# Kernel tuning notes

Measured on AMD Instinct MI355X. Metric: run time of the kernel, lower is better.

## Reference

```python
import jax, jax.numpy as jnp
import numpy as np

# LSNNParameters defaults (norse-style)
ALPHA = 100.0            # surrogate sharpness
DT = 1e-3
TAU_SYN_INV = 1.0 / 0.005   # 200
TAU_MEM_INV = 1.0 / 0.01    # 100
TAU_ADAPT_INV = 1.0 / 800.0
V_LEAK = 0.0
V_RESET = 0.0
BETA = 1.8
VTH = 1.0                # sp.vth_init / v_th default


@jax.custom_vjp
def superspike(x):
    # Heaviside forward, SuperSpike surrogate backward ('super' method)
    return (x > 0).astype(x.dtype)

def _ss_fwd(x):
    return superspike(x), x

def _ss_bwd(x, g):
    return (g / (ALPHA * jnp.abs(x) + 1.0) ** 2,)

superspike.defvjp(_ss_fwd, _ss_bwd)


def lsnn_scan(x, w_in, w_rec):
    # x: [T, B, N_in]; w_in: [H, N_in]; w_rec: [H, H]
    T, B, _ = x.shape
    H = w_in.shape[0]
    z0 = jnp.zeros((B, H), x.dtype)
    v0 = jnp.full((B, H), V_LEAK, x.dtype)
    i0 = jnp.zeros((B, H), x.dtype)
    b0 = jnp.full((B, H), VTH, x.dtype)  # mean(v_th)

    def step(carry, xt):
        z, v, i, b = carry
        v_dec = v + DT * TAU_MEM_INV * (V_LEAK - v + i)
        i_dec = i - DT * TAU_SYN_INV * i
        b_dec = b + DT * TAU_ADAPT_INV * (VTH - b)
        z_new = superspike(v_dec - b_dec)
        zd = jax.lax.stop_gradient(z_new)  # reset/adaptation use detached spike
        v_new = (1.0 - zd) * v_dec + zd * V_RESET
        i_new = i_dec + xt @ w_in.T + z @ w_rec.T
        b_new = b_dec + zd * BETA
        return (z_new, v_new, i_new, b_new), z_new

    (zf, vf, i_f, bf), outs = jax.lax.scan(step, (z0, v0, i0, b0), x)
    return outs, (zf, vf, i_f, bf)


def setup_inputs() -> dict:
    key = jax.random.key(0)
    k1, k2, k3 = jax.random.split(key, 3)
    T, B, N_IN, H = 512, 64, 512, 1024
    x = jax.random.normal(k1, (T, B, N_IN), jnp.float32)
    w_in = jax.random.normal(k2, (H, N_IN), jnp.float32) * np.float32(np.sqrt(2.0 / H))
    w_rec = jax.random.normal(k3, (H, H), jnp.float32) * np.float32(np.sqrt(2.0 / H))
    w_rec = w_rec * (1.0 - jnp.eye(H, dtype=jnp.float32))  # autapses=False
    return {"input_tensor": x, "input_weights": w_in, "recurrent_weights": w_rec}


def reference(input_tensor, input_weights, recurrent_weights):
    return lsnn_scan(input_tensor, input_weights, recurrent_weights)
```

## Files before the change

kernel.cpp:

```cpp
#include <hip/hip_runtime.h>

typedef float f32x4 __attribute__((ext_vector_type(4)));

#define T_STEPS 512
#define BATCH   64
#define NIN     512
#define H       1024
#define BH      (BATCH * H)

#define BM 128
#define BN 128
#define BK 16
#define LDSS 132

__global__ void transpose1024(const float* __restrict__ in, float* __restrict__ out) {
    __shared__ float tile[32][33];
    const int tx = threadIdx.x, ty = threadIdx.y;
    const int xg = blockIdx.x * 32 + tx;
    const int ybase = blockIdx.y * 32;
#pragma unroll
    for (int r = 0; r < 32; r += 8)
        tile[ty + r][tx] = in[(size_t)(ybase + ty + r) * H + xg];
    __syncthreads();
    const int x2 = blockIdx.y * 32 + tx;
    const int y2base = blockIdx.x * 32;
#pragma unroll
    for (int r = 0; r < 32; r += 8)
        out[(size_t)(y2base + ty + r) * H + x2] = tile[tx][ty + r];
}

__global__ __launch_bounds__(256) void gemm_xwin(const float* __restrict__ x,
                                                 const float* __restrict__ w,
                                                 float* __restrict__ cur) {
    __shared__ __align__(16) float As[BK][LDSS];
    __shared__ __align__(16) float Bs[BK][LDSS];
    const int tid = threadIdx.x;
    const int tx = tid & 15, ty = tid >> 4;
    const int tx4 = tx * 4, ty4 = ty * 4;
    const int m0 = blockIdx.y * BM;
    const int n0 = blockIdx.x * BN;

    float acc[8][8];
#pragma unroll
    for (int i = 0; i < 8; ++i)
#pragma unroll
        for (int j = 0; j < 8; ++j) acc[i][j] = 0.0f;

    const int ar = tid >> 2;
    const int akc = (tid & 3) * 4;

    float4 a0 = *reinterpret_cast<const float4*>(&x[(size_t)(m0 + ar) * NIN + akc]);
    float4 a1 = *reinterpret_cast<const float4*>(&x[(size_t)(m0 + ar + 64) * NIN + akc]);
    float4 b0 = *reinterpret_cast<const float4*>(&w[(size_t)(n0 + ar) * NIN + akc]);
    float4 b1 = *reinterpret_cast<const float4*>(&w[(size_t)(n0 + ar + 64) * NIN + akc]);

    for (int k0 = 0; k0 < NIN; k0 += BK) {
        __syncthreads();
        As[akc + 0][ar] = a0.x; As[akc + 1][ar] = a0.y; As[akc + 2][ar] = a0.z; As[akc + 3][ar] = a0.w;
        As[akc + 0][ar + 64] = a1.x; As[akc + 1][ar + 64] = a1.y; As[akc + 2][ar + 64] = a1.z; As[akc + 3][ar + 64] = a1.w;
        Bs[akc + 0][ar] = b0.x; Bs[akc + 1][ar] = b0.y; Bs[akc + 2][ar] = b0.z; Bs[akc + 3][ar] = b0.w;
        Bs[akc + 0][ar + 64] = b1.x; Bs[akc + 1][ar + 64] = b1.y; Bs[akc + 2][ar + 64] = b1.z; Bs[akc + 3][ar + 64] = b1.w;
        __syncthreads();

        const int kn = (k0 + BK < NIN) ? (k0 + BK) : 0;
        a0 = *reinterpret_cast<const float4*>(&x[(size_t)(m0 + ar) * NIN + kn + akc]);
        a1 = *reinterpret_cast<const float4*>(&x[(size_t)(m0 + ar + 64) * NIN + kn + akc]);
        b0 = *reinterpret_cast<const float4*>(&w[(size_t)(n0 + ar) * NIN + kn + akc]);
        b1 = *reinterpret_cast<const float4*>(&w[(size_t)(n0 + ar + 64) * NIN + kn + akc]);

#pragma unroll
        for (int kk = 0; kk < BK; ++kk) {
            const float4 av0 = *reinterpret_cast<const float4*>(&As[kk][ty4]);
            const float4 av1 = *reinterpret_cast<const float4*>(&As[kk][ty4 + 64]);
            const float4 bv0 = *reinterpret_cast<const float4*>(&Bs[kk][tx4]);
            const float4 bv1 = *reinterpret_cast<const float4*>(&Bs[kk][tx4 + 64]);
            const float ar_[8] = {av0.x, av0.y, av0.z, av0.w, av1.x, av1.y, av1.z, av1.w};
            const float br_[8] = {bv0.x, bv0.y, bv0.z, bv0.w, bv1.x, bv1.y, bv1.z, bv1.w};
#pragma unroll
            for (int i = 0; i < 8; ++i)
#pragma unroll
                for (int j = 0; j < 8; ++j)
                    acc[i][j] = fmaf(ar_[i], br_[j], acc[i][j]);
        }
    }

#pragma unroll
    for (int gi = 0; gi < 2; ++gi)
#pragma unroll
        for (int ii = 0; ii < 4; ++ii) {
            const int i = gi * 4 + ii;
            const int row = m0 + ty4 + ii + gi * 64;
            float* dst = &cur[(size_t)row * H + n0 + tx4];
            *reinterpret_cast<float4*>(dst)      = make_float4(acc[i][0], acc[i][1], acc[i][2], acc[i][3]);
            *reinterpret_cast<float4*>(dst + 64) = make_float4(acc[i][4], acc[i][5], acc[i][6], acc[i][7]);
        }
}

__global__ __launch_bounds__(256, 1) void lsnn_scan_kernel(float* __restrict__ io,
                                                           const float* __restrict__ wrecT) {
    const int tid = threadIdx.x;
    const int wave = tid >> 6, lane = tid & 63;
    const int j0 = tid * 4;
    const int wq = wave * 256;
    const int b = blockIdx.x;

    __shared__ __align__(16) float ring[3][4][1024];
    __shared__ __align__(16) int list[2][1088];
    __shared__ __align__(16) int cnt[2][4];

    float sv0 = 0.f, sv1 = 0.f, sv2 = 0.f, sv3 = 0.f;
    float si0 = 0.f, si1 = 0.f, si2 = 0.f, si3 = 0.f;
    float sb0 = 1.f, sb1 = 1.f, sb2 = 1.f, sb3 = 1.f;
    float sz0 = 0.f, sz1 = 0.f, sz2 = 0.f, sz3 = 0.f;
    int p = 0;
    int n_carry = 0;

    const float C_MEM = (float)(1e-3 * 100.0);
    const float C_SYN = (float)(1e-3 * 200.0);
    const float C_AD  = (float)(1e-3 * (1.0 / 800.0));
    const float BETA  = 1.8f;

    float* base = io + (size_t)b * H + j0;

    f32x4 P0 = *reinterpret_cast<const f32x4*>(base + (size_t)0 * BH);
    f32x4 P1 = *reinterpret_cast<const f32x4*>(base + (size_t)1 * BH);
    f32x4 P2 = *reinterpret_cast<const f32x4*>(base + (size_t)2 * BH);
    f32x4 P3 = *reinterpret_cast<const f32x4*>(base + (size_t)3 * BH);
    f32x4 P4 = *reinterpret_cast<const f32x4*>(base + (size_t)4 * BH);
    f32x4 P5 = *reinterpret_cast<const f32x4*>(base + (size_t)5 * BH);
    f32x4 P6 = *reinterpret_cast<const f32x4*>(base + (size_t)6 * BH);
    f32x4 P7 = *reinterpret_cast<const f32x4*>(base + (size_t)7 * BH);

#define STAGE(G, SLOT)                                                        \
  { const int A0s_ = (G) << 2;                                                \
    _Pragma("unroll")                                                         \
    for (int rr_ = 0; rr_ < 4; ++rr_) {                                       \
      const int ps_ = A0s_ + rr_;                                             \
      int hs_ = lst[ps_];                                                     \
      hs_ = (ps_ < n) ? hs_ : 0;                                              \
      const float* gp_ = wrecT + (size_t)(unsigned)hs_ * H + wq + lane * 4;   \
      __builtin_amdgcn_global_load_lds(                                       \
          (const __attribute__((address_space(1))) unsigned int*)gp_,         \
          (__attribute__((address_space(3))) unsigned int*)&ring[SLOT][rr_][wq], \
          16, 0, 0);                                                          \
    } }

#define SCAN_STEP(T, CREG, PF)                                                \
  {                                                                           \
    const float cc0 = CREG.x, cc1 = CREG.y, cc2 = CREG.z, cc3 = CREG.w;       \
    const int n = __builtin_amdgcn_readfirstlane(n_carry);                    \
    const int NT = (n + 3) >> 2;                                              \
    const int* lst = &list[p][0];                                             \
     \
    if (NT > 0) STAGE(0, 0);                                                  \
    if (NT > 1) STAGE(1, 1);                                                  \
    if (NT > 2) STAGE(2, 2);                                                  \
                                  \
    const float vd0 = sv0 + C_MEM * (0.0f - sv0 + si0);                       \
    const float vd1 = sv1 + C_MEM * (0.0f - sv1 + si1);                       \
    const float vd2 = sv2 + C_MEM * (0.0f - sv2 + si2);                       \
    const float vd3 = sv3 + C_MEM * (0.0f - sv3 + si3);                       \
    const float id0 = si0 - C_SYN * si0;                                      \
    const float id1 = si1 - C_SYN * si1;                                      \
    const float id2 = si2 - C_SYN * si2;                                      \
    const float id3 = si3 - C_SYN * si3;                                      \
    const float bd0 = sb0 + C_AD * (1.0f - sb0);                              \
    const float bd1 = sb1 + C_AD * (1.0f - sb1);                              \
    const float bd2 = sb2 + C_AD * (1.0f - sb2);                              \
    const float bd3 = sb3 + C_AD * (1.0f - sb3);                              \
    sz0 = ((vd0 - bd0) > 0.0f) ? 1.0f : 0.0f;                                 \
    sz1 = ((vd1 - bd1) > 0.0f) ? 1.0f : 0.0f;                                 \
    sz2 = ((vd2 - bd2) > 0.0f) ? 1.0f : 0.0f;                                 \
    sz3 = ((vd3 - bd3) > 0.0f) ? 1.0f : 0.0f;                                 \
    sv0 = (sz0 > 0.0f) ? 0.0f : vd0;                                          \
    sv1 = (sz1 > 0.0f) ? 0.0f : vd1;                                          \
    sv2 = (sz2 > 0.0f) ? 0.0f : vd2;                                          \
    sv3 = (sz3 > 0.0f) ? 0.0f : vd3;                                          \
    sb0 = (sz0 > 0.0f) ? (bd0 + BETA) : bd0;                                  \
    sb1 = (sz1 > 0.0f) ? (bd1 + BETA) : bd1;                                  \
    sb2 = (sz2 > 0.0f) ? (bd2 + BETA) : bd2;                                  \
    sb3 = (sz3 > 0.0f) ? (bd3 + BETA) : bd3;                                  \
    *reinterpret_cast<f32x4*>(base + (size_t)(T) * BH) =                      \
        (f32x4){sz0, sz1, sz2, sz3};                                          \
    const unsigned long long m0 = __ballot(sz0 > 0.0f);                       \
    const unsigned long long m1 = __ballot(sz1 > 0.0f);                       \
    const unsigned long long m2 = __ballot(sz2 > 0.0f);                       \
    const unsigned long long m3 = __ballot(sz3 > 0.0f);                       \
    unsigned pos = __builtin_amdgcn_mbcnt_hi((unsigned)(m0 >> 32),            \
                   __builtin_amdgcn_mbcnt_lo((unsigned)m0, 0u));              \
    pos = __builtin_amdgcn_mbcnt_hi((unsigned)(m1 >> 32),                     \
          __builtin_amdgcn_mbcnt_lo((unsigned)m1, pos));                      \
    pos = __builtin_amdgcn_mbcnt_hi((unsigned)(m2 >> 32),                     \
          __builtin_amdgcn_mbcnt_lo((unsigned)m2, pos));                      \
    pos = __builtin_amdgcn_mbcnt_hi((unsigned)(m3 >> 32),                     \
          __builtin_amdgcn_mbcnt_lo((unsigned)m3, pos));                      \
    if (lane == 0)                                                            \
      cnt[p ^ 1][wave] = __popcll(m0) + __popcll(m1) + __popcll(m2) + __popcll(m3); \
    asm volatile("s_waitcnt lgkmcnt(0)" ::: "memory");                        \
    __builtin_amdgcn_s_barrier();                                             \
    const int4 nc = *reinterpret_cast<const int4*>(&cnt[p ^ 1][0]);           \
    n_carry = nc.x + nc.y + nc.z + nc.w;                                      \
    const int woff = (wave > 0 ? nc.x : 0) + (wave > 1 ? nc.y : 0) +          \
                     (wave > 2 ? nc.z : 0);                                   \
    int* dst = &list[p ^ 1][woff];                                            \
    if (sz0 > 0.0f) dst[pos++] = j0 + 0;                                      \
    if (sz1 > 0.0f) dst[pos++] = j0 + 1;                                      \
    if (sz2 > 0.0f) dst[pos++] = j0 + 2;                                      \
    if (sz3 > 0.0f) dst[pos++] = j0 + 3;                                      \
    asm volatile("s_waitcnt lgkmcnt(0)" ::: "memory");                        \
    __builtin_amdgcn_s_barrier();                                             \
        \
    float r0 = 0.f, r1 = 0.f, r2 = 0.f, r3 = 0.f;                             \
    {                                                                         \
      int sl = 0;                                                             \
      for (int g = 0; g < NT; ++g) {                                          \
        const int rem = NT - 1 - g;                                           \
        if (rem >= 2)      { asm volatile("s_waitcnt vmcnt(8)" ::: "memory"); } \
        else if (rem == 1) { asm volatile("s_waitcnt vmcnt(4)" ::: "memory"); } \
        else               { asm volatile("s_waitcnt vmcnt(0)" ::: "memory"); } \
        const f32x4 w0 = *reinterpret_cast<const f32x4*>(&ring[sl][0][j0]);   \
        const f32x4 w1 = *reinterpret_cast<const f32x4*>(&ring[sl][1][j0]);   \
        const f32x4 w2 = *reinterpret_cast<const f32x4*>(&ring[sl][2][j0]);   \
        const f32x4 w3 = *reinterpret_cast<const f32x4*>(&ring[sl][3][j0]);   \
        const int gb = g << 2;                                                \
        if (gb + 4 <= n) {                                                    \
          r0 += w0.x; r1 += w0.y; r2 += w0.z; r3 += w0.w;                     \
          r0 += w1.x; r1 += w1.y; r2 += w1.z; r3 += w1.w;                     \
          r0 += w2.x; r1 += w2.y; r2 += w2.z; r3 += w2.w;                     \
          r0 += w3.x; r1 += w3.y; r2 += w3.z; r3 += w3.w;                     \
        } else {                                                              \
          const float ma_ = (gb + 0 < n) ? 1.0f : 0.0f;                       \
          r0 = fmaf(ma_, w0.x, r0); r1 = fmaf(ma_, w0.y, r1);                 \
          r2 = fmaf(ma_, w0.z, r2); r3 = fmaf(ma_, w0.w, r3);                 \
          const float mb_ = (gb + 1 < n) ? 1.0f : 0.0f;                       \
          r0 = fmaf(mb_, w1.x, r0); r1 = fmaf(mb_, w1.y, r1);                 \
          r2 = fmaf(mb_, w1.z, r2); r3 = fmaf(mb_, w1.w, r3);                 \
          const float mc_ = (gb + 2 < n) ? 1.0f : 0.0f;                       \
          r0 = fmaf(mc_, w2.x, r0); r1 = fmaf(mc_, w2.y, r1);                 \
          r2 = fmaf(mc_, w2.z, r2); r3 = fmaf(mc_, w2.w, r3);                 \
          const float md_ = (gb + 3 < n) ? 1.0f : 0.0f;                       \
          r0 = fmaf(md_, w3.x, r0); r1 = fmaf(md_, w3.y, r1);                 \
          r2 = fmaf(md_, w3.z, r2); r3 = fmaf(md_, w3.w, r3);                 \
        }                                                                     \
        if (g + 3 < NT) {                                                     \
             \
          asm volatile("s_waitcnt lgkmcnt(0)" ::: "memory");                  \
          STAGE(g + 3, sl);                                                   \
        }                                                                     \
        sl = (sl == 2) ? 0 : sl + 1;                                          \
      }                                                                       \
    }                                                                         \
    if (PF) {                                                                 \
      if ((T) + 1 < T_STEPS) {                                                \
        const float* pb = base + (size_t)((T) + 1) * BH;                      \
        P0 = *(const f32x4*)(pb + (size_t)0 * BH);                            \
        P1 = *(const f32x4*)(pb + (size_t)1 * BH);                            \
        P2 = *(const f32x4*)(pb + (size_t)2 * BH);                            \
        P3 = *(const f32x4*)(pb + (size_t)3 * BH);                            \
        P4 = *(const f32x4*)(pb + (size_t)4 * BH);                            \
        P5 = *(const f32x4*)(pb + (size_t)5 * BH);                            \
        P6 = *(const f32x4*)(pb + (size_t)6 * BH);                            \
        P7 = *(const f32x4*)(pb + (size_t)7 * BH);                            \
      }                                                                       \
    }                                                                         \
    si0 = (id0 + cc0) + r0;                                                   \
    si1 = (id1 + cc1) + r1;                                                   \
    si2 = (id2 + cc2) + r2;                                                   \
    si3 = (id3 + cc3) + r3;                                                   \
    p ^= 1;                                                                   \
  }

    for (int t = 0; t < T_STEPS; t += 8) {
        SCAN_STEP(t,     P0, 0);
        SCAN_STEP(t + 1, P1, 0);
        SCAN_STEP(t + 2, P2, 0);
        SCAN_STEP(t + 3, P3, 0);
        SCAN_STEP(t + 4, P4, 0);
        SCAN_STEP(t + 5, P5, 0);
        SCAN_STEP(t + 6, P6, 0);
        SCAN_STEP(t + 7, P7, 1);
    }
#undef SCAN_STEP
#undef STAGE

    float* fo = io + (size_t)T_STEPS * BH + (size_t)b * H + j0;
    *reinterpret_cast<float4*>(fo)          = make_float4(sz0, sz1, sz2, sz3);
    *reinterpret_cast<float4*>(fo + BH)     = make_float4(sv0, sv1, sv2, sv3);
    *reinterpret_cast<float4*>(fo + 2 * BH) = make_float4(si0, si1, si2, si3);
    *reinterpret_cast<float4*>(fo + 3 * BH) = make_float4(sb0, sb1, sb2, sb3);
}

extern "C" void kernel_launch(void* const* d_in, const int* in_sizes, int n_in,
                              void* d_out, int out_size, void* d_ws, size_t ws_size,
                              hipStream_t stream) {
    const float* x     = (const float*)d_in[0];
    const float* w_in  = (const float*)d_in[1];
    const float* w_rec = (const float*)d_in[2];
    float* out   = (float*)d_out;
    float* wrecT = (float*)d_ws;

    transpose1024<<<dim3(H / 32, H / 32), dim3(32, 8), 0, stream>>>(w_rec, wrecT);
    gemm_xwin<<<dim3(H / BN, (T_STEPS * BATCH) / BM), 256, 0, stream>>>(x, w_in, out);
    lsnn_scan_kernel<<<BATCH, 256, 0, stream>>>(out, wrecT);
}
```

Measured before the change: 747.9 us.

## Overlap tail of input GEMM with recurrent scan using persistent fused kernel

The input projection GEMM is split. The head covering the first 308 timesteps runs as before, and the remaining tiles are computed by extra blocks inside a fused kernel that also runs the 64 scan blocks. The scan reads the precomputed currents with agent-scope atomic loads and spins until the sentinel pattern that a memset writes beforehand has been overwritten. This is meant to hide the GEMM tail behind the latency-bound sequential scan. It adds a memset, polling overhead and a risk of deadlock or stale reads if the GEMM blocks are not co-resident. The LDS ring also grows from 3 to 4 slots, which removes the lgkmcnt wait before restaging.

```diff
diff --git a/kernel.cpp b/kernel.cpp
--- a/kernel.cpp
+++ b/kernel.cpp
@@ -7,11 +7,24 @@
 #define NIN     512
 #define H       1024
 #define BH      (BATCH * H)
+#define SENTU   0x7F7F7F7Fu
 
 #define BM 128
 #define BN 128
 #define BK 16
 #define LDSS 132
+
+#define T1S   308
+#define M1T   (T1S / 2)
+#define NI2   ((256 - M1T) * 8)
+#define PERS  384
+
+__device__ __forceinline__ float ld_agent(const float* p) {
+    return __hip_atomic_load(p, __ATOMIC_RELAXED, __HIP_MEMORY_SCOPE_AGENT);
+}
+__device__ __forceinline__ void st_agent(float* p, float v) {
+    __hip_atomic_store(p, v, __ATOMIC_RELAXED, __HIP_MEMORY_SCOPE_AGENT);
+}
 
 __global__ void transpose1024(const float* __restrict__ in, float* __restrict__ out) {
     __shared__ float tile[32][33];
@@ -29,7 +42,7 @@
         out[(size_t)(y2base + ty + r) * H + x2] = tile[tx][ty + r];
 }
 
-__global__ __launch_bounds__(256) void gemm_xwin(const float* __restrict__ x,
+__global__ __launch_bounds__(256) void gemm_head(const float* __restrict__ x,
                                                  const float* __restrict__ w,
                                                  float* __restrict__ cur) {
     __shared__ __align__(16) float As[BK][LDSS];
@@ -96,17 +109,98 @@
         }
 }
 
-__global__ __launch_bounds__(256, 1) void lsnn_scan_kernel(float* __restrict__ io,
-                                                           const float* __restrict__ wrecT) {
+__global__ void fused_tail(const float* __restrict__ x,
+                           const float* __restrict__ w,
+                           float* __restrict__ io,
+                           const float* __restrict__ wrecT) {
+    __shared__ __align__(16) char smem[4 * 4 * 1024 * 4 + 2 * 1088 * 4 + 32];
+
+    const int slot = blockIdx.x & 7;
+    if (slot >= 2) {
+        const int gp = blockIdx.x >> 3;
+        const int pb = gp * 6 + (slot - 2);
+        float* cur = io;
+
+        float (*As)[LDSS] = reinterpret_cast<float (*)[LDSS]>(smem);
+        float (*Bs)[LDSS] = reinterpret_cast<float (*)[LDSS]>(smem + BK * LDSS * sizeof(float));
+
+        const int tid = threadIdx.x;
+        const int tx = tid & 15, ty = tid >> 4;
+        const int tx4 = tx * 4, ty4 = ty * 4;
+        const int ar = tid >> 2;
+        const int akc = (tid & 3) * 4;
+
+        for (int wi = pb; wi < NI2; wi += PERS) {
+            const int m0 = (M1T + (wi >> 3)) * BM;
+            const int n0 = (wi & 7) * BN;
+
+            float acc[8][8];
+#pragma unroll
+            for (int i = 0; i < 8; ++i)
+#pragma unroll
+                for (int j = 0; j < 8; ++j) acc[i][j] = 0.0f;
+
+            float4 a0 = *reinterpret_cast<const float4*>(&x[(size_t)(m0 + ar) * NIN + akc]);
+            float4 a1 = *reinterpret_cast<const float4*>(&x[(size_t)(m0 + ar + 64) * NIN + akc]);
+            float4 b0 = *reinterpret_cast<const float4*>(&w[(size_t)(n0 + ar) * NIN + akc]);
+            float4 b1 = *reinterpret_cast<const float4*>(&w[(size_t)(n0 + ar + 64) * NIN + akc]);
+
+            for (int k0 = 0; k0 < NIN; k0 += BK) {
+                __syncthreads();
+                As[akc + 0][ar] = a0.x; As[akc + 1][ar] = a0.y; As[akc + 2][ar] = a0.z; As[akc + 3][ar] = a0.w;
+                As[akc + 0][ar + 64] = a1.x; As[akc + 1][ar + 64] = a1.y; As[akc + 2][ar + 64] = a1.z; As[akc + 3][ar + 64] = a1.w;
+                Bs[akc + 0][ar] = b0.x; Bs[akc + 1][ar] = b0.y; Bs[akc + 2][ar] = b0.z; Bs[akc + 3][ar] = b0.w;
+                Bs[akc + 0][ar + 64] = b1.x; Bs[akc + 1][ar + 64] = b1.y; Bs[akc + 2][ar + 64] = b1.z; Bs[akc + 3][ar + 64] = b1.w;
+                __syncthreads();
+
+                const int kn = (k0 + BK < NIN) ? (k0 + BK) : 0;
+                a0 = *reinterpret_cast<const float4*>(&x[(size_t)(m0 + ar) * NIN + kn + akc]);
+                a1 = *reinterpret_cast<const float4*>(&x[(size_t)(m0 + ar + 64) * NIN + kn + akc]);
+                b0 = *reinterpret_cast<const float4*>(&w[(size_t)(n0 + ar) * NIN + kn + akc]);
+                b1 = *reinterpret_cast<const float4*>(&w[(size_t)(n0 + ar + 64) * NIN + kn + akc]);
+
+#pragma unroll
+                for (int kk = 0; kk < BK; ++kk) {
+                    const float4 av0 = *reinterpret_cast<const float4*>(&As[kk][ty4]);
+                    const float4 av1 = *reinterpret_cast<const float4*>(&As[kk][ty4 + 64]);
+                    const float4 bv0 = *reinterpret_cast<const float4*>(&Bs[kk][tx4]);
+                    const float4 bv1 = *reinterpret_cast<const float4*>(&Bs[kk][tx4 + 64]);
+                    const float ar_[8] = {av0.x, av0.y, av0.z, av0.w, av1.x, av1.y, av1.z, av1.w};
+                    const float br_[8] = {bv0.x, bv0.y, bv0.z, bv0.w, bv1.x, bv1.y, bv1.z, bv1.w};
+#pragma unroll
+                    for (int i = 0; i < 8; ++i)
+#pragma unroll
+                        for (int j = 0; j < 8; ++j)
+                            acc[i][j] = fmaf(ar_[i], br_[j], acc[i][j]);
+                }
+            }
+
+#pragma unroll
+            for (int gi = 0; gi < 2; ++gi)
+#pragma unroll
+                for (int ii = 0; ii < 4; ++ii) {
+                    const int i = gi * 4 + ii;
+                    const int row = m0 + ty4 + ii + gi * 64;
+                    float* dst = &cur[(size_t)row * H + n0 + tx4];
+                    st_agent(dst + 0,  acc[i][0]); st_agent(dst + 1,  acc[i][1]);
+                    st_agent(dst + 2,  acc[i][2]); st_agent(dst + 3,  acc[i][3]);
+                    st_agent(dst + 64, acc[i][4]); st_agent(dst + 65, acc[i][5]);
+                    st_agent(dst + 66, acc[i][6]); st_agent(dst + 67, acc[i][7]);
+                }
+        }
+        return;
+    }
+
+    if (blockIdx.x >= 256) return;
+    const int b = (blockIdx.x >> 3) * 2 + slot;
     const int tid = threadIdx.x;
     const int wave = tid >> 6, lane = tid & 63;
     const int j0 = tid * 4;
     const int wq = wave * 256;
-    const int b = blockIdx.x;
-
-    __shared__ __align__(16) float ring[3][4][1024];
-    __shared__ __align__(16) int list[2][1088];
-    __shared__ __align__(16) int cnt[2][4];
+
+    float (*ring)[4][1024] = reinterpret_cast<float (*)[4][1024]>(smem);
+    int   (*list)[1088]    = reinterpret_cast<int (*)[1088]>(smem + 65536);
+    int   (*cnt)[4]        = reinterpret_cast<int (*)[4]>(smem + 65536 + 8704);
 
     float sv0 = 0.f, sv1 = 0.f, sv2 = 0.f, sv3 = 0.f;
     float si0 = 0.f, si1 = 0.f, si2 = 0.f, si3 = 0.f;
@@ -122,16 +216,35 @@
 
     float* base = io + (size_t)b * H + j0;
 
-    f32x4 P0 = *reinterpret_cast<const f32x4*>(base + (size_t)0 * BH);
-    f32x4 P1 = *reinterpret_cast<const f32x4*>(base + (size_t)1 * BH);
-    f32x4 P2 = *reinterpret_cast<const f32x4*>(base + (size_t)2 * BH);
-    f32x4 P3 = *reinterpret_cast<const f32x4*>(base + (size_t)3 * BH);
-    f32x4 P4 = *reinterpret_cast<const f32x4*>(base + (size_t)4 * BH);
-    f32x4 P5 = *reinterpret_cast<const f32x4*>(base + (size_t)5 * BH);
-    f32x4 P6 = *reinterpret_cast<const f32x4*>(base + (size_t)6 * BH);
-    f32x4 P7 = *reinterpret_cast<const f32x4*>(base + (size_t)7 * BH);
-
-#define STAGE(G, SLOT)                                                        \
+    if (lane == 0) cnt[0][wave] = 0;
+    asm volatile("s_waitcnt lgkmcnt(0)" ::: "memory");
+    __builtin_amdgcn_s_barrier();
+
+    f32x4 P0, P1, P2, P3, P4, P5, P6, P7;
+
+#define LDP(REG, KK)                                                          \
+      REG.x = ld_agent(pb_ + (size_t)(KK) * BH + 0);                          \
+      REG.y = ld_agent(pb_ + (size_t)(KK) * BH + 1);                          \
+      REG.z = ld_agent(pb_ + (size_t)(KK) * BH + 2);                          \
+      REG.w = ld_agent(pb_ + (size_t)(KK) * BH + 3);                          \
+      bad_ |= (unsigned)(__float_as_uint(REG.x) == SENTU);                    \
+      bad_ |= (unsigned)(__float_as_uint(REG.y) == SENTU);                    \
+      bad_ |= (unsigned)(__float_as_uint(REG.z) == SENTU);                    \
+      bad_ |= (unsigned)(__float_as_uint(REG.w) == SENTU);
+
+#define LOADP8_SPIN(PBASE)                                                    \
+  { const float* pb_ = (PBASE);                                               \
+    for (int tries_ = 0; tries_ < (1 << 14); ++tries_) {                      \
+      unsigned bad_ = 0u;                                                     \
+      LDP(P0, 0) LDP(P1, 1) LDP(P2, 2) LDP(P3, 3)                             \
+      LDP(P4, 4) LDP(P5, 5) LDP(P6, 6) LDP(P7, 7)                             \
+      if (__ballot(bad_ != 0u) == 0ull) break;                                \
+      __builtin_amdgcn_s_sleep(8);                                            \
+    } }
+
+    LOADP8_SPIN(base);
+
+#define STAGE(G)                                                              \
   { const int A0s_ = (G) << 2;                                                \
     _Pragma("unroll")                                                         \
     for (int rr_ = 0; rr_ < 4; ++rr_) {                                       \
@@ -141,7 +254,7 @@
       const float* gp_ = wrecT + (size_t)(unsigned)hs_ * H + wq + lane * 4;   \
       __builtin_amdgcn_global_load_lds(                                       \
           (const __attribute__((address_space(1))) unsigned int*)gp_,         \
-          (__attribute__((address_space(3))) unsigned int*)&ring[SLOT][rr_][wq], \
+          (__attribute__((address_space(3))) unsigned int*)&ring[(G) & 3][rr_][wq], \
           16, 0, 0);                                                          \
     } }
 
@@ -151,11 +264,9 @@
     const int n = __builtin_amdgcn_readfirstlane(n_carry);                    \
     const int NT = (n + 3) >> 2;                                              \
     const int* lst = &list[p][0];                                             \
-     \
-    if (NT > 0) STAGE(0, 0);                                                  \
-    if (NT > 1) STAGE(1, 1);                                                  \
-    if (NT > 2) STAGE(2, 2);                                                  \
-                                  \
+    if (NT > 0) STAGE(0);                                                     \
+    if (NT > 1) STAGE(1);                                                     \
+    if (NT > 2) STAGE(2);                                                     \
     const float vd0 = sv0 + C_MEM * (0.0f - sv0 + si0);                       \
     const float vd1 = sv1 + C_MEM * (0.0f - sv1 + si1);                       \
     const float vd2 = sv2 + C_MEM * (0.0f - sv2 + si2);                       \
@@ -209,15 +320,14 @@
     if (sz3 > 0.0f) dst[pos++] = j0 + 3;                                      \
     asm volatile("s_waitcnt lgkmcnt(0)" ::: "memory");                        \
     __builtin_amdgcn_s_barrier();                                             \
-        \
     float r0 = 0.f, r1 = 0.f, r2 = 0.f, r3 = 0.f;                             \
     {                                                                         \
-      int sl = 0;                                                             \
       for (int g = 0; g < NT; ++g) {                                          \
         const int rem = NT - 1 - g;                                           \
         if (rem >= 2)      { asm volatile("s_waitcnt vmcnt(8)" ::: "memory"); } \
         else if (rem == 1) { asm volatile("s_waitcnt vmcnt(4)" ::: "memory"); } \
         else               { asm volatile("s_waitcnt vmcnt(0)" ::: "memory"); } \
+        const int sl = g & 3;                                                 \
         const f32x4 w0 = *reinterpret_cast<const f32x4*>(&ring[sl][0][j0]);   \
         const f32x4 w1 = *reinterpret_cast<const f32x4*>(&ring[sl][1][j0]);   \
         const f32x4 w2 = *reinterpret_cast<const f32x4*>(&ring[sl][2][j0]);   \
@@ -242,25 +352,12 @@
           r0 = fmaf(md_, w3.x, r0); r1 = fmaf(md_, w3.y, r1);                 \
           r2 = fmaf(md_, w3.z, r2); r3 = fmaf(md_, w3.w, r3);                 \
         }                                                                     \
-        if (g + 3 < NT) {                                                     \
-             \
-          asm volatile("s_waitcnt lgkmcnt(0)" ::: "memory");                  \
-          STAGE(g + 3, sl);                                                   \
-        }                                                                     \
-        sl = (sl == 2) ? 0 : sl + 1;                                          \
+        if (g + 3 < NT) STAGE(g + 3);                                         \
       }                                                                       \
     }                                                                         \
     if (PF) {                                                                 \
       if ((T) + 1 < T_STEPS) {                                                \
-        const float* pb = base + (size_t)((T) + 1) * BH;                      \
-        P0 = *(const f32x4*)(pb + (size_t)0 * BH);                            \
-        P1 = *(const f32x4*)(pb + (size_t)1 * BH);                            \
-        P2 = *(const f32x4*)(pb + (size_t)2 * BH);                            \
-        P3 = *(const f32x4*)(pb + (size_t)3 * BH);                            \
-        P4 = *(const f32x4*)(pb + (size_t)4 * BH);                            \
-        P5 = *(const f32x4*)(pb + (size_t)5 * BH);                            \
-        P6 = *(const f32x4*)(pb + (size_t)6 * BH);                            \
-        P7 = *(const f32x4*)(pb + (size_t)7 * BH);                            \
+        LOADP8_SPIN(base + (size_t)((T) + 1) * BH);                           \
       }                                                                       \
     }                                                                         \
     si0 = (id0 + cc0) + r0;                                                   \
@@ -282,6 +379,8 @@
     }
 #undef SCAN_STEP
 #undef STAGE
+#undef LOADP8_SPIN
+#undef LDP
 
     float* fo = io + (size_t)T_STEPS * BH + (size_t)b * H + j0;
     *reinterpret_cast<float4*>(fo)          = make_float4(sz0, sz1, sz2, sz3);
@@ -299,7 +398,9 @@
     float* out   = (float*)d_out;
     float* wrecT = (float*)d_ws;
 
+    hipMemsetAsync(out + (size_t)T1S * BH, 0x7F,
+                   (size_t)(T_STEPS - T1S) * BH * sizeof(float), stream);
     transpose1024<<<dim3(H / 32, H / 32), dim3(32, 8), 0, stream>>>(w_rec, wrecT);
-    gemm_xwin<<<dim3(H / BN, (T_STEPS * BATCH) / BM), 256, 0, stream>>>(x, w_in, out);
-    lsnn_scan_kernel<<<BATCH, 256, 0, stream>>>(out, wrecT);
-}
+    gemm_head<<<dim3(H / BN, (T1S * BATCH) / BM), 256, 0, stream>>>(x, w_in, out);
+    fused_tail<<<dim3(64 * 8), 256, 0, stream>>>(x, w_in, out, wrecT);
+}
```

Result: slower. 811.8 us (+8.5%).
